# Kernel tuning notes

Measured on AMD Instinct MI355X. Metric: run time of the kernel, lower is better.

## Reference

```python
import jax, jax.numpy as jnp
import numpy as np

EMB = 2048
HEADS = 16


def setup_inputs() -> dict:
    key = jax.random.key(0)
    k_x, k_wqkv, k_bqkv, k_wo, k_bo = jax.random.split(key, 5)
    B, S, E = 2, 2048, EMB
    x = jax.random.normal(k_x, (B, S, E), dtype=jnp.float32)
    # nn.Linear weights stored as (in, out) for x @ W + b convention
    W_qkv = jax.random.normal(k_wqkv, (E, 3 * E), dtype=jnp.float32) * 0.02
    b_qkv = jax.random.normal(k_bqkv, (3 * E,), dtype=jnp.float32) * 0.02
    W_out = jax.random.normal(k_wo, (E, E), dtype=jnp.float32) * 0.02
    b_out = jax.random.normal(k_bo, (E,), dtype=jnp.float32) * 0.02
    return {"x": x, "W_qkv": W_qkv, "b_qkv": b_qkv, "W_out": W_out, "b_out": b_out}


def reference(x, W_qkv, b_qkv, W_out, b_out):
    B, S, E = x.shape
    H = HEADS
    dh = E // H
    # QKV projection: (B,S,3E)
    qkv = x @ W_qkv + b_qkv
    # Faithful to torch: reshape (B,S,H,3*dh) THEN split -> interleaved per-head q/k/v
    qkv = qkv.reshape(B, S, H, 3 * dh).transpose(0, 2, 1, 3)  # (B,H,S,3*dh)
    q, k, v = jnp.split(qkv, 3, axis=-1)  # each (B,H,S,dh)
    q = q / jnp.asarray(dh, q.dtype) ** 0.5
    scores = jnp.einsum('bhqd,bhkd->bhqk', q, k)  # (B,H,S,S)
    weights = jax.nn.softmax(scores, axis=-1)
    attn = jnp.einsum('bhqk,bhkd->bhqd', weights, v)  # (B,H,S,dh)
    attn = attn.transpose(0, 2, 1, 3).reshape(B, S, E)
    return attn @ W_out + b_out
```

## Files before the change

kernel.cpp:

```cpp
#include <hip/hip_runtime.h>
#include <type_traits>
#include <utility>

#define DI __device__ __forceinline__

typedef unsigned short u16;
typedef float f32x4 __attribute__((ext_vector_type(4)));
typedef float f32x16 __attribute__((ext_vector_type(16)));
typedef short s16x8 __attribute__((ext_vector_type(8)));
typedef __bf16 bf16x8 __attribute__((ext_vector_type(8)));

template <typename V, typename = void>
struct mfma_ok : std::false_type {};
template <typename V>
struct mfma_ok<V, std::void_t<decltype(__builtin_amdgcn_mfma_f32_16x16x32_bf16(
    std::declval<V>(), std::declval<V>(), std::declval<f32x4>(), 0, 0, 0))>>
    : std::true_type {};
using frag_t = std::conditional_t<mfma_ok<bf16x8>::value, bf16x8, s16x8>;

union U128 {
  int4 i;
  frag_t f;
  u16 s[8];
};

DI f32x4 mfma16(const U128& a, const U128& b, f32x4 c) {
  return __builtin_amdgcn_mfma_f32_16x16x32_bf16(a.f, b.f, c, 0, 0, 0);
}
DI f32x16 mfma32(const U128& a, const U128& b, f32x16 c) {
  return __builtin_amdgcn_mfma_f32_32x32x16_bf16(a.f, b.f, c, 0, 0, 0);
}

DI u16 f2b(float x) {
  union { float f; unsigned u; } v; v.f = x;
  unsigned r = v.u + 0x7FFFu + ((v.u >> 16) & 1u);
  return (u16)(r >> 16);
}

DI unsigned pk2bf(float a, float b) {
  unsigned short ua = __builtin_bit_cast(unsigned short, (__bf16)a);
  unsigned short ub = __builtin_bit_cast(unsigned short, (__bf16)b);
  return (unsigned)ua | ((unsigned)ub << 16);
}

#if __has_builtin(__builtin_amdgcn_exp2f)
#define EXP2F __builtin_amdgcn_exp2f
#else
#define EXP2F exp2f
#endif

DI void plswap(unsigned& lo, unsigned& hi) {
  asm("v_permlane32_swap_b32 %0, %1" : "+v"(lo), "+v"(hi));
}

typedef __attribute__((address_space(1))) void gas_t;
typedef __attribute__((address_space(3))) void las_t;
DI void gll16(const void* g, void* l) {
  __builtin_amdgcn_global_load_lds((gas_t*)g, (las_t*)l, 16, 0, 0);
}

#define QSCALE 0.12751791437603762f

DI void transpose_tile(const float* __restrict__ in, u16* __restrict__ out,
                       int R, int C, int bx, int by, int t, u16 (*Tb)[68]) {
  long r0 = (long)by * 64, c0 = (long)bx * 64;
  int cq = (t & 15) * 4, rr = t >> 4;
#pragma unroll
  for (int it = 0; it < 4; ++it) {
    int r = rr + it * 16;
    float4 v = *(const float4*)(in + (r0 + r) * C + c0 + cq);
    Tb[r][cq + 0] = f2b(v.x); Tb[r][cq + 1] = f2b(v.y);
    Tb[r][cq + 2] = f2b(v.z); Tb[r][cq + 3] = f2b(v.w);
  }
  __syncthreads();
#pragma unroll
  for (int it = 0; it < 2; ++it) {
    int ci = it * 256 + t;
    int cc = ci >> 3, ch = ci & 7, rb = ch * 8;
    unsigned p0 = Tb[rb + 0][cc] | ((unsigned)Tb[rb + 1][cc] << 16);
    unsigned p1 = Tb[rb + 2][cc] | ((unsigned)Tb[rb + 3][cc] << 16);
    unsigned p2 = Tb[rb + 4][cc] | ((unsigned)Tb[rb + 5][cc] << 16);
    unsigned p3 = Tb[rb + 6][cc] | ((unsigned)Tb[rb + 7][cc] << 16);
    *(int4*)(out + (c0 + cc) * R + r0 + rb) = make_int4(p0, p1, p2, p3);
  }
}

__global__ __launch_bounds__(256) void k_pre(const float* __restrict__ x,
                                             u16* __restrict__ xb,
                                             const float* __restrict__ Wqkv,
                                             u16* __restrict__ wqkvt) {
  __shared__ __attribute__((aligned(16))) u16 Tb[64][68];
  int bid = blockIdx.x, t = threadIdx.x;
  if (bid < 8192) {
    int i = bid * 256 + t;
    float4 v = ((const float4*)x)[i];
    ushort4 o;
    o.x = f2b(v.x); o.y = f2b(v.y); o.z = f2b(v.z); o.w = f2b(v.w);
    ((ushort4*)xb)[i] = o;
    return;
  }
  int idx = bid - 8192;
  transpose_tile(Wqkv, wqkvt, 2048, 6144, idx % 96, idx / 96, t, Tb);
}

template <int MODE>
__global__ __launch_bounds__(256, 4) void k_gemm_bt(const u16* __restrict__ A,
                                                    const u16* __restrict__ Bt,
                                                    const float* __restrict__ bias,
                                                    void* __restrict__ Cout,
                                                    u16* __restrict__ qb,
                                                    u16* __restrict__ kbv,
                                                    u16* __restrict__ vt,
                                                    int n_off,
                                                    int M, int N, int K) {
  __shared__ __attribute__((aligned(16))) u16 SM[16640];
  u16* As = SM;
  u16* Bs = SM + 8192;
  int t = threadIdx.x;
  int lane = t & 63, w = t >> 6, quad = lane >> 4, l15 = lane & 15;
  long m0 = (long)blockIdx.y * 128, n0 = n_off + (long)blockIdx.x * 128;
  int wr = (w >> 1) * 64, wc = (w & 1) * 64;
  int sw = l15 & 7;
  f32x4 acc[4][4] = {};
  for (int k0 = 0; k0 < K; k0 += 64) {
    __syncthreads();
#pragma unroll
    for (int it = 0; it < 4; ++it) {
      int ci = it * 256 + t;
      int row = ci >> 3, cl = (ci & 7) ^ (row & 7);
      gll16(A + (m0 + row) * K + k0 + cl * 8, As + ci * 8);
      gll16(Bt + (n0 + row) * K + k0 + cl * 8, Bs + ci * 8);
    }
    __syncthreads();
#pragma unroll
    for (int kk = 0; kk < 2; ++kk) {
      U128 a[4], b[4];
#pragma unroll
      for (int i = 0; i < 4; ++i)
        a[i].i = *(const int4*)(As + (wr + i * 16 + l15) * 64 + (((kk * 4 + quad) ^ sw) << 3));
#pragma unroll
      for (int j = 0; j < 4; ++j)
        b[j].i = *(const int4*)(Bs + (wc + j * 16 + l15) * 64 + (((kk * 4 + quad) ^ sw) << 3));
#pragma unroll
      for (int i = 0; i < 4; ++i)
#pragma unroll
        for (int j = 0; j < 4; ++j)
          acc[i][j] = mfma16(a[i], b[j], acc[i][j]);
    }
  }
  float bj[4];
#pragma unroll
  for (int j = 0; j < 4; ++j) bj[j] = bias[n0 + wc + j * 16 + l15];

  int hidx = (int)(n0 / 384);
  int rsel = (int)(n0 - hidx * 384) >> 7;

  if (MODE == 1 && rsel == 2) {
    __syncthreads();
#pragma unroll
    for (int i = 0; i < 4; ++i)
#pragma unroll
      for (int rr2 = 0; rr2 < 4; ++rr2) {
        int m = wr + i * 16 + quad * 4 + rr2;
#pragma unroll
        for (int j = 0; j < 4; ++j)
          SM[(wc + j * 16 + l15) * 130 + m] = f2b(acc[i][j][rr2] + bj[j]);
      }
    __syncthreads();
    int bidx = (int)(m0 >> 11);
    int stile = (int)((m0 & 2047) >> 7);
    u16* vtile = vt + (long)(bidx * 16 + hidx) * 262144 + stile * 16384;
    const unsigned* sm32 = (const unsigned*)SM;
#pragma unroll
    for (int it = 0; it < 8; ++it) {
      int ci = it * 256 + t;
      int d = ci >> 4, sb = (ci & 15) * 8;
      int base = (d * 130 + sb) >> 1;
      *(int4*)(vtile + d * 128 + sb) =
          make_int4(sm32[base], sm32[base + 1], sm32[base + 2], sm32[base + 3]);
    }
    return;
  }

  u16* route = (MODE == 1) ? (rsel == 0 ? qb : kbv) : nullptr;

#pragma unroll
  for (int i = 0; i < 4; ++i) {
#pragma unroll
    for (int rr2 = 0; rr2 < 4; ++rr2) {
      long row = m0 + wr + i * 16 + quad * 4 + rr2;
#pragma unroll
      for (int j = 0; j < 4; ++j) {
        float v = acc[i][j][rr2] + bj[j];
        if (MODE == 1) {
          if (rsel == 0) v *= QSCALE;
          int bidx = (int)(row >> 11), s = (int)(row & 2047);
          long obase = ((long)(bidx * 16 + hidx) * 2048 + s) * 128;
          int dh = wc + j * 16 + l15;
          unsigned pb = f2b(v);
          unsigned other = __shfl_xor(pb, 1);
          if (!(l15 & 1))
            ((unsigned*)route)[(obase + dh) >> 1] = pb | (other << 16);
        } else {
          long col = n0 + wc + j * 16 + l15;
          unsigned bits = __float_as_uint(v);
          unsigned other = __shfl_xor(bits, 1);
          if (!(l15 & 1)) {
            uint2 pr; pr.x = bits; pr.y = other;
            *(uint2*)((float*)Cout + row * N + col) = pr;
          }
        }
      }
    }
  }
}

__global__ __launch_bounds__(512, 2) void k_flash(const u16* __restrict__ qb,
                                                  const u16* __restrict__ kb,
                                                  const u16* __restrict__ vt,
                                                  u16* __restrict__ attn,
                                                  const float* __restrict__ Wout,
                                                  u16* __restrict__ woutt) {
  __shared__ __attribute__((aligned(16))) u16 Ks[2][64 * 128];
  __shared__ __attribute__((aligned(16))) u16 Vts[2][128 * 64];
  if (blockIdx.y >= 32) {
    int half = threadIdx.x >> 8, tt = threadIdx.x & 255;
    u16 (*Tb)[68] = (u16(*)[68])(&Ks[0][0] + half * 64 * 68);
    int u = ((blockIdx.y - 32) * 8 + blockIdx.x) * 2 + half;
    transpose_tile(Wout, woutt, 2048, 2048, u & 31, u >> 5, tt, Tb);
    return;
  }
  int t = threadIdx.x;
  int lane = t & 63, w = t >> 6, l31 = lane & 31, h = lane >> 5;
  int d0 = blockIdx.y * 8 + blockIdx.x;
  int bh = (d0 & 7) + ((d0 >> 6) << 3);
  int jq = (d0 >> 3) & 7;
  int q0 = jq * 256 + w * 32;
  int b = bh >> 4, hd = bh & 15;

  const u16* qbase = qb + ((long)bh * 2048 + q0 + l31) * 128;
  U128 qf[8];
#pragma unroll
  for (int dht = 0; dht < 8; ++dht)
    qf[dht].i = *(const int4*)(qbase + dht * 16 + h * 8);
  __syncthreads();

  f32x16 O[4] = {};
  float ls0 = 0.f, ls1 = 0.f, ls2 = 0.f, ls3 = 0.f;
  const u16* kbh = kb + (long)bh * 2048 * 128;
  long vbase = (long)bh * 262144;

  unsigned swx = (unsigned)(((l31 & 7) << 3) ^ (h << 3));
  unsigned kinv = ((unsigned)l31 << 7) ^ swx;
  unsigned vinv = ((unsigned)l31 << 6) ^ swx;

  auto stage = [&](int buf, int k0) {
#pragma unroll
    for (int it = 0; it < 2; ++it) {
      int ci = it * 512 + t;
      int key = ci >> 4, cp = ci & 15, cl = cp ^ (key & 7);
      gll16(kbh + (long)(k0 + key) * 128 + cl * 8, &Ks[buf][0] + ci * 8);
    }
#pragma unroll
    for (int it = 0; it < 2; ++it) {
      int ci = it * 512 + t;
      int d = ci >> 3, cp = ci & 7, cl = cp ^ (d & 7);
      gll16(vt + vbase + ((k0 >> 7) << 14) + d * 128 + (k0 & 64) + cl * 8,
            &Vts[buf][0] + ci * 8);
    }
  };

  stage(0, 0);
  int cur = 0;
  for (int k0 = 0; k0 < 2048; k0 += 64) {
    if (k0 + 64 < 2048) {
      stage(cur ^ 1, k0 + 64);
      asm volatile("s_waitcnt vmcnt(4)" ::: "memory");
    } else {
      asm volatile("s_waitcnt vmcnt(0)" ::: "memory");
    }
    __builtin_amdgcn_s_barrier();
    asm volatile("" ::: "memory");
    const u16* KbT = &Ks[cur][0];
    const u16* VbT = &Vts[cur][0];

    f32x16 St0 = {}, St1 = {};
    __builtin_amdgcn_s_setprio(1);
#pragma unroll
    for (int dht = 0; dht < 8; ++dht) {
      U128 kf;
      kf.i = *(const int4*)(KbT + (kinv ^ (unsigned)(dht << 4)));
      St0 = mfma32(kf, qf[dht], St0);
    }
#pragma unroll
    for (int dht = 0; dht < 8; ++dht) {
      U128 kf;
      kf.i = *(const int4*)(KbT + (kinv ^ (unsigned)(dht << 4)) + 4096);
      St1 = mfma32(kf, qf[dht], St1);
    }
    __builtin_amdgcn_s_setprio(0);

    auto pv = [&](int kt, const U128& pfk) {
#pragma unroll
      for (int dht = 0; dht < 4; ++dht) {
        U128 vf;
        vf.i = *(const int4*)(VbT + (vinv ^ (unsigned)(kt << 4)) + dht * 2048);
        O[dht] = mfma32(vf, pfk, O[dht]);
      }
    };
    auto mkpf = [&](const float* p) {
      unsigned w0 = pk2bf(p[0], p[1]);
      unsigned w1 = pk2bf(p[2], p[3]);
      unsigned w2 = pk2bf(p[4], p[5]);
      unsigned w3 = pk2bf(p[6], p[7]);
      plswap(w0, w2);
      plswap(w1, w3);
      U128 r; r.i = make_int4(w0, w1, w2, w3);
      return r;
    };

    float p0[16];
#pragma unroll
    for (int r = 0; r < 16; r += 4) {
      p0[r + 0] = EXP2F(St0[r + 0]); ls0 += p0[r + 0];
      p0[r + 1] = EXP2F(St0[r + 1]); ls1 += p0[r + 1];
      p0[r + 2] = EXP2F(St0[r + 2]); ls2 += p0[r + 2];
      p0[r + 3] = EXP2F(St0[r + 3]); ls3 += p0[r + 3];
    }
    U128 pf0 = mkpf(&p0[0]);
    U128 pf1 = mkpf(&p0[8]);

    pv(0, pf0);

    float p1[16];
#pragma unroll
    for (int r = 0; r < 8; r += 4) {
      p1[r + 0] = EXP2F(St1[r + 0]); ls0 += p1[r + 0];
      p1[r + 1] = EXP2F(St1[r + 1]); ls1 += p1[r + 1];
      p1[r + 2] = EXP2F(St1[r + 2]); ls2 += p1[r + 2];
      p1[r + 3] = EXP2F(St1[r + 3]); ls3 += p1[r + 3];
    }
    pv(1, pf1);

#pragma unroll
    for (int r = 8; r < 16; r += 4) {
      p1[r + 0] = EXP2F(St1[r + 0]); ls0 += p1[r + 0];
      p1[r + 1] = EXP2F(St1[r + 1]); ls1 += p1[r + 1];
      p1[r + 2] = EXP2F(St1[r + 2]); ls2 += p1[r + 2];
      p1[r + 3] = EXP2F(St1[r + 3]); ls3 += p1[r + 3];
    }
    U128 pf2 = mkpf(&p1[0]);
    U128 pf3 = mkpf(&p1[8]);

    __builtin_amdgcn_s_setprio(1);
    pv(2, pf2);
    pv(3, pf3);
    __builtin_amdgcn_s_setprio(0);

    asm volatile("" ::: "memory");
    __builtin_amdgcn_s_barrier();
    cur ^= 1;
  }

  float lsum = (ls0 + ls1) + (ls2 + ls3);
  float ltot = lsum + __shfl_xor(lsum, 32);
  float inv = 1.f / ltot;
  long orow = (long)b * 2048 + q0 + l31;
  u16* ob = attn + orow * 2048 + hd * 128;
#pragma unroll
  for (int dht = 0; dht < 4; ++dht)
#pragma unroll
    for (int g = 0; g < 4; ++g) {
      int dh = dht * 32 + g * 8 + h * 4;
      float v0 = O[dht][4 * g + 0] * inv, v1 = O[dht][4 * g + 1] * inv;
      float v2 = O[dht][4 * g + 2] * inv, v3 = O[dht][4 * g + 3] * inv;
      uint2 pkd;
      pkd.x = pk2bf(v0, v1);
      pkd.y = pk2bf(v2, v3);
      *(uint2*)(ob + dh) = pkd;
    }
}

extern "C" void kernel_launch(void* const* d_in, const int* in_sizes, int n_in,
                              void* d_out, int out_size, void* d_ws, size_t ws_size,
                              hipStream_t stream) {
  const float* x    = (const float*)d_in[0];
  const float* Wqkv = (const float*)d_in[1];
  const float* bqkv = (const float*)d_in[2];
  const float* Wout = (const float*)d_in[3];
  const float* bout = (const float*)d_in[4];
  float* out = (float*)d_out;
  char* ws = (char*)d_ws;

  if (ws_size < 75497472u) return;

  u16* xb    = (u16*)d_out;
  u16* wqkvt = (u16*)(ws);
  u16* qbuf  = (u16*)(ws + 25165824);
  u16* kbuf  = (u16*)(ws + 41943040);
  u16* vtb   = (u16*)(ws + 58720256);
  u16* woutt = (u16*)(ws);
  u16* attnb = (u16*)(ws + 8388608);

  k_pre<<<11264, 256, 0, stream>>>(x, xb, Wqkv, wqkvt);
  k_gemm_bt<1><<<dim3(48, 32), 256, 0, stream>>>(xb, wqkvt, bqkv, nullptr,
                                                 qbuf, kbuf, vtb, 0, 4096, 6144, 2048);
  k_flash<<<dim3(8, 96), 512, 0, stream>>>(qbuf, kbuf, vtb, attnb, Wout, woutt);
  k_gemm_bt<0><<<dim3(16, 32), 256, 0, stream>>>(attnb, woutt, bout, out,
                                                 nullptr, nullptr, nullptr, 0, 4096, 2048, 2048);
}
```

Measured before the change: 370.9 us.

## Double flash attention key tile to 128 and halve transpose blocks

The flash attention kernel now stages 128 keys per iteration instead of 64. K and V^T shared buffers grow to 128x128 per stage, so there are half as many barriers and loop iterations, and the V layout matches the K swizzle. The Wout transpose blocks each handle two tiles, which shrinks the grid's extra rows from 64 to 32. Shared memory doubles to 128KB per block, which will likely drop occupancy from two blocks per CU to one, and fewer transpose blocks means less parallelism for that side work.

Measured after the change: 355.5 us. 1.04x faster.

```diff
diff --git a/kernel.cpp b/kernel.cpp
--- a/kernel.cpp
+++ b/kernel.cpp
@@ -221,13 +221,18 @@
                                                   u16* __restrict__ attn,
                                                   const float* __restrict__ Wout,
                                                   u16* __restrict__ woutt) {
-  __shared__ __attribute__((aligned(16))) u16 Ks[2][64 * 128];
-  __shared__ __attribute__((aligned(16))) u16 Vts[2][128 * 64];
+  __shared__ __attribute__((aligned(16))) u16 Ks[2][128 * 128];
+  __shared__ __attribute__((aligned(16))) u16 Vts[2][128 * 128];
   if (blockIdx.y >= 32) {
     int half = threadIdx.x >> 8, tt = threadIdx.x & 255;
     u16 (*Tb)[68] = (u16(*)[68])(&Ks[0][0] + half * 64 * 68);
-    int u = ((blockIdx.y - 32) * 8 + blockIdx.x) * 2 + half;
-    transpose_tile(Wout, woutt, 2048, 2048, u & 31, u >> 5, tt, Tb);
+    int ub = ((blockIdx.y - 32) * 8 + blockIdx.x) * 4 + half * 2;
+#pragma unroll
+    for (int rep = 0; rep < 2; ++rep) {
+      int u = ub + rep;
+      transpose_tile(Wout, woutt, 2048, 2048, u & 31, u >> 5, tt, Tb);
+      __syncthreads();
+    }
     return;
   }
   int t = threadIdx.x;
@@ -250,32 +255,30 @@
   const u16* kbh = kb + (long)bh * 2048 * 128;
   long vbase = (long)bh * 262144;
 
-  unsigned swx = (unsigned)(((l31 & 7) << 3) ^ (h << 3));
-  unsigned kinv = ((unsigned)l31 << 7) ^ swx;
-  unsigned vinv = ((unsigned)l31 << 6) ^ swx;
+  unsigned kinv = ((unsigned)l31 << 7) ^ (unsigned)(((l31 & 7) << 3) ^ (h << 3));
 
   auto stage = [&](int buf, int k0) {
 #pragma unroll
-    for (int it = 0; it < 2; ++it) {
+    for (int it = 0; it < 4; ++it) {
       int ci = it * 512 + t;
       int key = ci >> 4, cp = ci & 15, cl = cp ^ (key & 7);
       gll16(kbh + (long)(k0 + key) * 128 + cl * 8, &Ks[buf][0] + ci * 8);
     }
 #pragma unroll
-    for (int it = 0; it < 2; ++it) {
+    for (int it = 0; it < 4; ++it) {
       int ci = it * 512 + t;
-      int d = ci >> 3, cp = ci & 7, cl = cp ^ (d & 7);
-      gll16(vt + vbase + ((k0 >> 7) << 14) + d * 128 + (k0 & 64) + cl * 8,
+      int d = ci >> 4, cp = ci & 15, cl = cp ^ (d & 7);
+      gll16(vt + vbase + ((long)(k0 >> 7) << 14) + d * 128 + cl * 8,
             &Vts[buf][0] + ci * 8);
     }
   };
 
   stage(0, 0);
   int cur = 0;
-  for (int k0 = 0; k0 < 2048; k0 += 64) {
-    if (k0 + 64 < 2048) {
-      stage(cur ^ 1, k0 + 64);
-      asm volatile("s_waitcnt vmcnt(4)" ::: "memory");
+  for (int k0 = 0; k0 < 2048; k0 += 128) {
+    if (k0 + 128 < 2048) {
+      stage(cur ^ 1, k0 + 128);
+      asm volatile("s_waitcnt vmcnt(8)" ::: "memory");
     } else {
       asm volatile("s_waitcnt vmcnt(0)" ::: "memory");
     }
@@ -284,19 +287,20 @@
     const u16* KbT = &Ks[cur][0];
     const u16* VbT = &Vts[cur][0];
 
-    f32x16 St0 = {}, St1 = {};
+    f32x16 St0 = {}, St1 = {}, St2 = {}, St3 = {};
     __builtin_amdgcn_s_setprio(1);
 #pragma unroll
     for (int dht = 0; dht < 8; ++dht) {
-      U128 kf;
-      kf.i = *(const int4*)(KbT + (kinv ^ (unsigned)(dht << 4)));
-      St0 = mfma32(kf, qf[dht], St0);
-    }
-#pragma unroll
-    for (int dht = 0; dht < 8; ++dht) {
-      U128 kf;
-      kf.i = *(const int4*)(KbT + (kinv ^ (unsigned)(dht << 4)) + 4096);
-      St1 = mfma32(kf, qf[dht], St1);
+      unsigned ka = kinv ^ (unsigned)(dht << 4);
+      U128 k0f, k1f, k2f, k3f;
+      k0f.i = *(const int4*)(KbT + ka);
+      k1f.i = *(const int4*)(KbT + ka + 4096);
+      k2f.i = *(const int4*)(KbT + ka + 8192);
+      k3f.i = *(const int4*)(KbT + ka + 12288);
+      St0 = mfma32(k0f, qf[dht], St0);
+      St1 = mfma32(k1f, qf[dht], St1);
+      St2 = mfma32(k2f, qf[dht], St2);
+      St3 = mfma32(k3f, qf[dht], St3);
     }
     __builtin_amdgcn_s_setprio(0);
 
@@ -304,7 +308,7 @@
 #pragma unroll
       for (int dht = 0; dht < 4; ++dht) {
         U128 vf;
-        vf.i = *(const int4*)(VbT + (vinv ^ (unsigned)(kt << 4)) + dht * 2048);
+        vf.i = *(const int4*)(VbT + dht * 4096 + (kinv ^ (unsigned)(kt << 4)));
         O[dht] = mfma32(vf, pfk, O[dht]);
       }
     };
@@ -318,44 +322,41 @@
       U128 r; r.i = make_int4(w0, w1, w2, w3);
       return r;
     };
-
-    float p0[16];
-#pragma unroll
-    for (int r = 0; r < 16; r += 4) {
-      p0[r + 0] = EXP2F(St0[r + 0]); ls0 += p0[r + 0];
-      p0[r + 1] = EXP2F(St0[r + 1]); ls1 += p0[r + 1];
-      p0[r + 2] = EXP2F(St0[r + 2]); ls2 += p0[r + 2];
-      p0[r + 3] = EXP2F(St0[r + 3]); ls3 += p0[r + 3];
-    }
-    U128 pf0 = mkpf(&p0[0]);
-    U128 pf1 = mkpf(&p0[8]);
-
-    pv(0, pf0);
-
-    float p1[16];
-#pragma unroll
-    for (int r = 0; r < 8; r += 4) {
-      p1[r + 0] = EXP2F(St1[r + 0]); ls0 += p1[r + 0];
-      p1[r + 1] = EXP2F(St1[r + 1]); ls1 += p1[r + 1];
-      p1[r + 2] = EXP2F(St1[r + 2]); ls2 += p1[r + 2];
-      p1[r + 3] = EXP2F(St1[r + 3]); ls3 += p1[r + 3];
-    }
-    pv(1, pf1);
-
-#pragma unroll
-    for (int r = 8; r < 16; r += 4) {
-      p1[r + 0] = EXP2F(St1[r + 0]); ls0 += p1[r + 0];
-      p1[r + 1] = EXP2F(St1[r + 1]); ls1 += p1[r + 1];
-      p1[r + 2] = EXP2F(St1[r + 2]); ls2 += p1[r + 2];
-      p1[r + 3] = EXP2F(St1[r + 3]); ls3 += p1[r + 3];
-    }
-    U128 pf2 = mkpf(&p1[0]);
-    U128 pf3 = mkpf(&p1[8]);
-
+#define SM8(St, p, off)                                        \
+    {                                                          \
+      p[off + 0] = EXP2F(St[off + 0]); ls0 += p[off + 0];      \
+      p[off + 1] = EXP2F(St[off + 1]); ls1 += p[off + 1];      \
+      p[off + 2] = EXP2F(St[off + 2]); ls2 += p[off + 2];      \
+      p[off + 3] = EXP2F(St[off + 3]); ls3 += p[off + 3];      \
+      p[off + 4] = EXP2F(St[off + 4]); ls0 += p[off + 4];      \
+      p[off + 5] = EXP2F(St[off + 5]); ls1 += p[off + 5];      \
+      p[off + 6] = EXP2F(St[off + 6]); ls2 += p[off + 6];      \
+      p[off + 7] = EXP2F(St[off + 7]); ls3 += p[off + 7];      \
+    }
+
+    float p0[16], p1[16], p2[16], p3[16];
+    SM8(St0, p0, 0) SM8(St0, p0, 8)
+    U128 pf0a = mkpf(&p0[0]), pf0b = mkpf(&p0[8]);
+    pv(0, pf0a);
+    SM8(St1, p1, 0)
+    pv(1, pf0b);
+    SM8(St1, p1, 8)
+    U128 pf1a = mkpf(&p1[0]), pf1b = mkpf(&p1[8]);
+    pv(2, pf1a);
+    SM8(St2, p2, 0)
+    pv(3, pf1b);
+    SM8(St2, p2, 8)
+    U128 pf2a = mkpf(&p2[0]), pf2b = mkpf(&p2[8]);
+    pv(4, pf2a);
+    SM8(St3, p3, 0)
+    pv(5, pf2b);
+    SM8(St3, p3, 8)
+    U128 pf3a = mkpf(&p3[0]), pf3b = mkpf(&p3[8]);
     __builtin_amdgcn_s_setprio(1);
-    pv(2, pf2);
-    pv(3, pf3);
+    pv(6, pf3a);
+    pv(7, pf3b);
     __builtin_amdgcn_s_setprio(0);
+#undef SM8
 
     asm volatile("" ::: "memory");
     __builtin_amdgcn_s_barrier();
@@ -405,7 +406,7 @@
   k_pre<<<11264, 256, 0, stream>>>(x, xb, Wqkv, wqkvt);
   k_gemm_bt<1><<<dim3(48, 32), 256, 0, stream>>>(xb, wqkvt, bqkv, nullptr,
                                                  qbuf, kbuf, vtb, 0, 4096, 6144, 2048);
-  k_flash<<<dim3(8, 96), 512, 0, stream>>>(qbuf, kbuf, vtb, attnb, Wout, woutt);
+  k_flash<<<dim3(8, 64), 512, 0, stream>>>(qbuf, kbuf, vtb, attnb, Wout, woutt);
   k_gemm_bt<0><<<dim3(16, 32), 256, 0, stream>>>(attnb, woutt, bout, out,
                                                  nullptr, nullptr, nullptr, 0, 4096, 2048, 2048);
 }
```
